# Kernel optimization log

Hardware: AMD Instinct MI355X
Metric: run time of the kernel (lower is better)

## Reference

```python
import jax, jax.numpy as jnp
import numpy as np

EMBED = 2048
MLP = 8192
EPS = 1e-5


def setup_inputs() -> dict:
    key = jax.random.key(0)
    ks = jax.random.split(key, 16)
    s = 0.02
    inp = {
        "x": jax.random.normal(ks[0], (2, 2048, EMBED), dtype=jnp.float32),
        "wq": jax.random.normal(ks[1], (EMBED, EMBED), dtype=jnp.float32) * s,
        "bq": jnp.zeros((EMBED,), jnp.float32),
        "wk": jax.random.normal(ks[2], (EMBED, EMBED), dtype=jnp.float32) * s,
        "bk": jnp.zeros((EMBED,), jnp.float32),
        "wv": jax.random.normal(ks[3], (EMBED, EMBED), dtype=jnp.float32) * s,
        "bv": jnp.zeros((EMBED,), jnp.float32),
        "wd": jax.random.normal(ks[4], (EMBED, EMBED), dtype=jnp.float32) * s,
        "bd": jnp.zeros((EMBED,), jnp.float32),
        "ln_g": jnp.ones((EMBED,), jnp.float32),
        "ln_b": jnp.zeros((EMBED,), jnp.float32),
        "w1": jax.random.normal(ks[5], (MLP, EMBED), dtype=jnp.float32) * s,
        "b1": jnp.zeros((MLP,), jnp.float32),
        "w2": jax.random.normal(ks[6], (EMBED, MLP), dtype=jnp.float32) * s,
        "b2": jnp.zeros((EMBED,), jnp.float32),
    }
    return inp


def _layernorm(x, g, b):
    mu = jnp.mean(x, axis=-1, keepdims=True)
    var = jnp.mean(jnp.square(x - mu), axis=-1, keepdims=True)
    return (x - mu) * jax.lax.rsqrt(var + EPS) * g + b


def reference(x, wq, bq, wk, bk, wv, bv, wd, bd, ln_g, ln_b, w1, b1, w2, b2):
    # Single-head attention; scale uses full embed_dim (rotary_emb.dim == embed_dim).
    q = jnp.einsum("bse,fe->bsf", x, wq) + bq
    k = jnp.einsum("bse,fe->bsf", x, wk) + bk
    v = jnp.einsum("bse,fe->bsf", x, wv) + bv
    scores = jnp.einsum("bqe,bke->bqk", q, k) / jnp.sqrt(jnp.float32(EMBED))
    probs = jax.nn.softmax(scores, axis=-1)
    ctx = jnp.einsum("bqk,bke->bqe", probs, v)
    attn_out = jnp.einsum("bse,fe->bsf", ctx, wd) + bd
    # residual (dropout is identity in eval mode)
    h = x + attn_out
    h = _layernorm(h, ln_g, ln_b)
    mlp = jnp.einsum("bse,fe->bsf", h, w1) + b1
    mlp = jax.nn.gelu(mlp, approximate=False)
    mlp = jnp.einsum("bsf,ef->bse", mlp, w2) + b2
    return h + mlp
```

## Files before the change

kernel.cpp:

```cpp
#include <hip/hip_runtime.h>
#include <math.h>


#define SEQ 2048
#define EMB 2048
#define MLPD 8192

typedef __attribute__((ext_vector_type(8))) short short8;
typedef __attribute__((ext_vector_type(4))) float floatx4;
typedef unsigned short ushort;

__device__ __forceinline__ short f2bf(float f) {
  union { float f; unsigned u; } v; v.f = f;
  unsigned r = v.u + 0x7FFFu + ((v.u >> 16) & 1u);
  return (short)(r >> 16);
}

__device__ __forceinline__ void gload16(const ushort* g, ushort* l) {
  __builtin_amdgcn_global_load_lds(
      (__attribute__((address_space(1))) void*)g,
      (__attribute__((address_space(3))) void*)(unsigned)(unsigned long)l,
      16, 0, 0);
}

enum { EPI_QKV = 0, EPI_SCORES = 1, EPI_PV = 2, EPI_RES = 3, EPI_GELU = 4 };

template<int EPI>
__global__ __launch_bounds__(512, 2)
void gemm256(const ushort* __restrict__ A, const ushort* __restrict__ B,
             const float* __restrict__ bias, void* __restrict__ Cp,
             int N, int K, int lda, int ldb, int ldc,
             long sA, long sB, long sC, float scale)
{
  extern __shared__ ushort lds[];
  const int t = threadIdx.x;
  const int lane = t & 63, w = t >> 6;
  const int wm = w >> 2, wn = w & 3;
  const long bm = (long)blockIdx.y * 256;
  const long bn = (long)blockIdx.x * 256;
  A += (long)blockIdx.z * sA;
  B += (long)blockIdx.z * sB;

  const int srow = (w << 3) + (lane >> 3);
  const int gcol = (lane & 7) ^ ((lane >> 3) & 7);
  const ushort* Ag = A + (bm + srow) * (long)lda + gcol * 8;
  const ushort* Bg = B + (bn + srow) * (long)ldb + gcol * 8;
  ushort* lw = lds + (w << 9);

#define STAGE(gb, ld, dst, kk) do {                         \
    const ushort* _g = (gb) + (kk);                         \
    gload16(_g, lw + (dst));                                \
    gload16(_g + 64L * (ld), lw + (dst) + 4096); } while (0)

  const int l15 = lane & 15, q = lane >> 4, swz = l15 & 7;
  const int kx0 = (q ^ swz) << 3;
  const int kx1 = ((4 + q) ^ swz) << 3;
  const int arow = (wm << 13) + l15 * 64;
  const int brow = 16384 + ((wn >> 1) << 13) + ((wn & 1) << 12) + l15 * 64;

  floatx4 acc[8][4];
#pragma unroll
  for (int m = 0; m < 8; ++m)
#pragma unroll
    for (int n = 0; n < 4; ++n) acc[m][n] = (floatx4)0.0f;

  const int NT = K >> 6;

  STAGE(Ag,              lda, 0,     0);
  STAGE(Ag + 128L * lda, lda, 8192,  0);
  STAGE(Bg,              ldb, 16384, 0);
  STAGE(Bg + 128L * ldb, ldb, 24576, 0);
  STAGE(Ag,              lda, 32768, 64);
  asm volatile("s_waitcnt vmcnt(2)" ::: "memory");
  __builtin_amdgcn_s_barrier();

  for (int kt = 0; kt < NT; ++kt) {
    const int buf  = (kt & 1) ? 32768 : 0;
    const int bufn = 32768 - buf;
    const long k1 = (long)((kt + 1 < NT) ? kt + 1 : NT - 1) << 6;
    const long k2 = (long)((kt + 2 < NT) ? kt + 2 : NT - 1) << 6;
    short8 a0[4], a1[4], b0[4], b1[4];

#pragma unroll
    for (int mf = 0; mf < 4; ++mf) {
      a0[mf] = *(const short8*)&lds[buf + arow + mf * 1024 + kx0];
      a1[mf] = *(const short8*)&lds[buf + arow + mf * 1024 + kx1];
    }
#pragma unroll
    for (int nf = 0; nf < 2; ++nf) {
      b0[nf] = *(const short8*)&lds[buf + brow + nf * 1024 + kx0];
      b1[nf] = *(const short8*)&lds[buf + brow + nf * 1024 + kx1];
    }
    STAGE(Ag + 128L * lda, lda, bufn + 8192, k1);
    __builtin_amdgcn_s_barrier();
    asm volatile("s_waitcnt lgkmcnt(0)");
    __builtin_amdgcn_s_setprio(1);
#pragma unroll
    for (int mf = 0; mf < 4; ++mf)
#pragma unroll
      for (int nf = 0; nf < 2; ++nf) {
        acc[mf][nf] = __builtin_amdgcn_mfma_f32_16x16x32_bf16(a0[mf], b0[nf], acc[mf][nf], 0, 0, 0);
        acc[mf][nf] = __builtin_amdgcn_mfma_f32_16x16x32_bf16(a1[mf], b1[nf], acc[mf][nf], 0, 0, 0);
      }
    __builtin_amdgcn_s_setprio(0);
    __builtin_amdgcn_s_barrier();

#pragma unroll
    for (int nf = 2; nf < 4; ++nf) {
      b0[nf] = *(const short8*)&lds[buf + brow + nf * 1024 + kx0];
      b1[nf] = *(const short8*)&lds[buf + brow + nf * 1024 + kx1];
    }
    STAGE(Bg, ldb, bufn + 16384, k1);
    __builtin_amdgcn_s_barrier();
    asm volatile("s_waitcnt lgkmcnt(0)");
    __builtin_amdgcn_s_setprio(1);
#pragma unroll
    for (int mf = 0; mf < 4; ++mf)
#pragma unroll
      for (int nf = 2; nf < 4; ++nf) {
        acc[mf][nf] = __builtin_amdgcn_mfma_f32_16x16x32_bf16(a0[mf], b0[nf], acc[mf][nf], 0, 0, 0);
        acc[mf][nf] = __builtin_amdgcn_mfma_f32_16x16x32_bf16(a1[mf], b1[nf], acc[mf][nf], 0, 0, 0);
      }
    __builtin_amdgcn_s_setprio(0);
    __builtin_amdgcn_s_barrier();

#pragma unroll
    for (int mf = 0; mf < 4; ++mf) {
      a0[mf] = *(const short8*)&lds[buf + arow + (4 + mf) * 1024 + kx0];
      a1[mf] = *(const short8*)&lds[buf + arow + (4 + mf) * 1024 + kx1];
    }
    STAGE(Bg + 128L * ldb, ldb, bufn + 24576, k1);
    __builtin_amdgcn_s_barrier();
    asm volatile("s_waitcnt lgkmcnt(0)");
    __builtin_amdgcn_s_setprio(1);
#pragma unroll
    for (int mf = 0; mf < 4; ++mf)
#pragma unroll
      for (int nf = 0; nf < 2; ++nf) {
        acc[4 + mf][nf] = __builtin_amdgcn_mfma_f32_16x16x32_bf16(a0[mf], b0[nf], acc[4 + mf][nf], 0, 0, 0);
        acc[4 + mf][nf] = __builtin_amdgcn_mfma_f32_16x16x32_bf16(a1[mf], b1[nf], acc[4 + mf][nf], 0, 0, 0);
      }
    __builtin_amdgcn_s_setprio(0);
    __builtin_amdgcn_s_barrier();

    STAGE(Ag, lda, buf, k2);
    __builtin_amdgcn_s_barrier();
    __builtin_amdgcn_s_setprio(1);
#pragma unroll
    for (int mf = 0; mf < 4; ++mf)
#pragma unroll
      for (int nf = 2; nf < 4; ++nf) {
        acc[4 + mf][nf] = __builtin_amdgcn_mfma_f32_16x16x32_bf16(a0[mf], b0[nf], acc[4 + mf][nf], 0, 0, 0);
        acc[4 + mf][nf] = __builtin_amdgcn_mfma_f32_16x16x32_bf16(a1[mf], b1[nf], acc[4 + mf][nf], 0, 0, 0);
      }
    __builtin_amdgcn_s_setprio(0);
    asm volatile("s_waitcnt vmcnt(2)" ::: "memory");
    __builtin_amdgcn_s_barrier();
  }
#undef STAGE

  const int lq = lane >> 4;
#pragma unroll
  for (int mf = 0; mf < 8; ++mf) {
#pragma unroll
    for (int nf = 0; nf < 4; ++nf) {
#pragma unroll
      for (int i = 0; i < 4; ++i) {
        const long r = bm + wm * 128 + mf * 16 + lq * 4 + i;
        const long c = bn + wn * 64 + nf * 16 + l15;
        float val = acc[mf][nf][i];
        if constexpr (EPI == EPI_QKV) {
          val += bias[c];
          ((ushort*)Cp)[r * (long)ldc + c] = (ushort)f2bf(val);
        } else if constexpr (EPI == EPI_SCORES) {
          ((float*)Cp)[(long)blockIdx.z * sC + r * (long)ldc + c] = val * scale;
        } else {
          val += bias[c];
          float g = 0.5f * val * (1.0f + erff(val * 0.70710678118f));
          ((ushort*)Cp)[r * (long)ldc + c] = (ushort)f2bf(g);
        }
      }
    }
  }
}

template<int EPI>
__global__ __launch_bounds__(256)
void gemm_bt(const ushort* __restrict__ A, const ushort* __restrict__ B,
             const float* __restrict__ bias, const float* __restrict__ res,
             void* __restrict__ Cp, int N, int K,
             int lda, int ldb, int ldc,
             long sA, long sB, long sC, float scale)
{
  __shared__ ushort As[128 * 32];
  __shared__ ushort Bs[128 * 32];

  const int t = threadIdx.x;
  const int lane = t & 63, wid = t >> 6;
  const int wm = wid >> 1, wn = wid & 1;
  const long bm = (long)blockIdx.y * 128;
  const long bn = (long)blockIdx.x * 128;
  A += (long)blockIdx.z * sA;
  B += (long)blockIdx.z * sB;

  const int srow = (wid << 5) + (lane >> 2);
  const int scol = (lane & 3) << 3;
  const ushort* a0 = A + (bm + srow) * (long)lda + scol;
  const ushort* a1 = a0 + 16L * lda;
  const ushort* b0 = B + (bn + srow) * (long)ldb + scol;
  const ushort* b1 = b0 + 16L * ldb;
  ushort* lA0 = As + (wid << 10);
  ushort* lA1 = lA0 + 512;
  ushort* lB0 = Bs + (wid << 10);
  ushort* lB1 = lB0 + 512;

  floatx4 acc[4][4];
#pragma unroll
  for (int m = 0; m < 4; ++m)
#pragma unroll
    for (int n = 0; n < 4; ++n) acc[m][n] = (floatx4)0.0f;

  const int l15 = lane & 15, kq = (lane >> 4) << 3;
  const int abase = ((wm << 6) + l15) * 32 + kq;
  const int bbase = ((wn << 6) + l15) * 32 + kq;

  for (int kb = 0; kb < K; kb += 32) {
    gload16(a0 + kb, lA0);
    gload16(a1 + kb, lA1);
    gload16(b0 + kb, lB0);
    gload16(b1 + kb, lB1);
    __syncthreads();

    short8 a[4], b[4];
#pragma unroll
    for (int m = 0; m < 4; ++m)
      a[m] = *reinterpret_cast<const short8*>(&As[abase + m * (16 * 32)]);
#pragma unroll
    for (int n = 0; n < 4; ++n)
      b[n] = *reinterpret_cast<const short8*>(&Bs[bbase + n * (16 * 32)]);
#pragma unroll
    for (int m = 0; m < 4; ++m)
#pragma unroll
      for (int n = 0; n < 4; ++n)
        acc[m][n] = __builtin_amdgcn_mfma_f32_16x16x32_bf16(a[m], b[n], acc[m][n], 0, 0, 0);
    __syncthreads();
  }

  const int lq = lane >> 4;
#pragma unroll
  for (int m = 0; m < 4; ++m) {
#pragma unroll
    for (int n = 0; n < 4; ++n) {
#pragma unroll
      for (int i = 0; i < 4; ++i) {
        const long r = bm + wm * 64 + m * 16 + lq * 4 + i;
        const long c = bn + wn * 64 + n * 16 + l15;
        float val = acc[m][n][i];
        if constexpr (EPI == EPI_SCORES) {
          ((float*)Cp)[(long)blockIdx.z * sC + r * (long)ldc + c] = val * scale;
        } else if constexpr (EPI == EPI_PV) {
          ((ushort*)Cp)[(long)blockIdx.z * sC + r * (long)ldc + c] = (ushort)f2bf(val);
        }
      }
    }
  }
}

__global__ __launch_bounds__(256)
void reduce2(const float* __restrict__ p0, const float* __restrict__ p1,
             const float* __restrict__ bias, const float* __restrict__ res,
             float* __restrict__ out)
{
  const long i = ((long)blockIdx.x * 256 + threadIdx.x) * 8;
  const int c = (int)(i & 2047);
  float4 a0 = *(const float4*)(p0 + i),  a1 = *(const float4*)(p0 + i + 4);
  float4 q0 = *(const float4*)(p1 + i),  q1 = *(const float4*)(p1 + i + 4);
  float4 r0 = *(const float4*)(res + i), r1 = *(const float4*)(res + i + 4);
  float4 b0 = *(const float4*)(bias + c), b1 = *(const float4*)(bias + c + 4);
  float4 o0 = {a0.x + q0.x + r0.x + b0.x, a0.y + q0.y + r0.y + b0.y,
               a0.z + q0.z + r0.z + b0.z, a0.w + q0.w + r0.w + b0.w};
  float4 o1 = {a1.x + q1.x + r1.x + b1.x, a1.y + q1.y + r1.y + b1.y,
               a1.z + q1.z + r1.z + b1.z, a1.w + q1.w + r1.w + b1.w};
  *(float4*)(out + i) = o0;
  *(float4*)(out + i + 4) = o1;
}

__global__ __launch_bounds__(256)
void cvt8(const float* __restrict__ s, ushort* __restrict__ d) {
  const long i = ((long)blockIdx.x * 256 + threadIdx.x) * 8;
  float4 a = *reinterpret_cast<const float4*>(s + i);
  float4 b = *reinterpret_cast<const float4*>(s + i + 4);
  short8 v;
  v[0] = f2bf(a.x); v[1] = f2bf(a.y); v[2] = f2bf(a.z); v[3] = f2bf(a.w);
  v[4] = f2bf(b.x); v[5] = f2bf(b.y); v[6] = f2bf(b.z); v[7] = f2bf(b.w);
  *reinterpret_cast<short8*>(d + i) = v;
}

__global__ __launch_bounds__(256)
void concat3(const float* __restrict__ b0, const float* __restrict__ b1,
             const float* __restrict__ b2, float* __restrict__ dst) {
  const int i = blockIdx.x * 256 + threadIdx.x;
  dst[i] = (i < 2048) ? b0[i] : (i < 4096) ? b1[i - 2048] : b2[i - 4096];
}

__global__ __launch_bounds__(256)
void transpose_v(const ushort* __restrict__ qkv, ushort* __restrict__ vT) {
  __shared__ ushort tile[32][33];
  const int b = blockIdx.z;
  const int s0 = blockIdx.x * 32, e0 = blockIdx.y * 32;
  const int tx = threadIdx.x & 31, ty = threadIdx.x >> 5;
#pragma unroll
  for (int i = 0; i < 4; ++i) {
    const long s = (long)b * SEQ + s0 + ty + i * 8;
    tile[ty + i * 8][tx] = qkv[s * 6144 + 4096 + e0 + tx];
  }
  __syncthreads();
#pragma unroll
  for (int i = 0; i < 4; ++i) {
    const long e = (long)b * SEQ + e0 + ty + i * 8;
    vT[e * SEQ + s0 + tx] = tile[tx][ty + i * 8];
  }
}

__global__ __launch_bounds__(256)
void softmax_rows(const float* __restrict__ S, ushort* __restrict__ P) {
  const long row = blockIdx.x;
  const float* src = S + row * 2048;
  const int t = threadIdx.x, lane = t & 63, wid = t >> 6;
  float4 a = *reinterpret_cast<const float4*>(src + t * 8);
  float4 b = *reinterpret_cast<const float4*>(src + t * 8 + 4);
  float v[8] = {a.x, a.y, a.z, a.w, b.x, b.y, b.z, b.w};
  float m = v[0];
#pragma unroll
  for (int i = 1; i < 8; ++i) m = fmaxf(m, v[i]);
#pragma unroll
  for (int o = 32; o; o >>= 1) m = fmaxf(m, __shfl_xor(m, o));
  __shared__ float rm[4], rs[4];
  if (!lane) rm[wid] = m;
  __syncthreads();
  m = fmaxf(fmaxf(rm[0], rm[1]), fmaxf(rm[2], rm[3]));
  float e[8], s = 0.f;
#pragma unroll
  for (int i = 0; i < 8; ++i) { e[i] = __expf(v[i] - m); s += e[i]; }
#pragma unroll
  for (int o = 32; o; o >>= 1) s += __shfl_xor(s, o);
  if (!lane) rs[wid] = s;
  __syncthreads();
  s = rs[0] + rs[1] + rs[2] + rs[3];
  const float inv = 1.0f / s;
  short8 wv;
#pragma unroll
  for (int i = 0; i < 8; ++i) wv[i] = f2bf(e[i] * inv);
  *reinterpret_cast<short8*>(P + row * 2048 + t * 8) = wv;
}

__global__ __launch_bounds__(256)
void layernorm_rows(const float* __restrict__ X, const float* __restrict__ g,
                    const float* __restrict__ bb, float* __restrict__ H,
                    ushort* __restrict__ Hb) {
  const long row = blockIdx.x;
  const float* src = X + row * 2048;
  const int t = threadIdx.x, lane = t & 63, wid = t >> 6;
  float4 a = *reinterpret_cast<const float4*>(src + t * 8);
  float4 b = *reinterpret_cast<const float4*>(src + t * 8 + 4);
  float v[8] = {a.x, a.y, a.z, a.w, b.x, b.y, b.z, b.w};
  float s = 0.f, ss = 0.f;
#pragma unroll
  for (int i = 0; i < 8; ++i) { s += v[i]; ss += v[i] * v[i]; }
#pragma unroll
  for (int o = 32; o; o >>= 1) { s += __shfl_xor(s, o); ss += __shfl_xor(ss, o); }
  __shared__ float r1[4], r2[4];
  if (!lane) { r1[wid] = s; r2[wid] = ss; }
  __syncthreads();
  s = r1[0] + r1[1] + r1[2] + r1[3];
  ss = r2[0] + r2[1] + r2[2] + r2[3];
  const float mu = s * (1.0f / 2048.0f);
  const float var = ss * (1.0f / 2048.0f) - mu * mu;
  const float inv = rsqrtf(var + 1e-5f);
  float o0[8];
  short8 wv;
#pragma unroll
  for (int i = 0; i < 8; ++i) {
    const int c = t * 8 + i;
    o0[i] = (v[i] - mu) * inv * g[c] + bb[c];
    wv[i] = f2bf(o0[i]);
  }
  float4 w0 = {o0[0], o0[1], o0[2], o0[3]}, w1 = {o0[4], o0[5], o0[6], o0[7]};
  *reinterpret_cast<float4*>(H + row * 2048 + t * 8) = w0;
  *reinterpret_cast<float4*>(H + row * 2048 + t * 8 + 4) = w1;
  *reinterpret_cast<short8*>(Hb + row * 2048 + t * 8) = wv;
}

extern "C" void kernel_launch(void* const* d_in, const int* in_sizes, int n_in,
                              void* d_out, int out_size, void* d_ws, size_t ws_size,
                              hipStream_t stream) {
  const float* x    = (const float*)d_in[0];
  const float* wq   = (const float*)d_in[1];
  const float* bq   = (const float*)d_in[2];
  const float* wk   = (const float*)d_in[3];
  const float* bk   = (const float*)d_in[4];
  const float* wv   = (const float*)d_in[5];
  const float* bv   = (const float*)d_in[6];
  const float* wd   = (const float*)d_in[7];
  const float* bd   = (const float*)d_in[8];
  const float* ln_g = (const float*)d_in[9];
  const float* ln_b = (const float*)d_in[10];
  const float* w1   = (const float*)d_in[11];
  const float* b1   = (const float*)d_in[12];
  const float* w2   = (const float*)d_in[13];
  const float* b2   = (const float*)d_in[14];
  float* out = (float*)d_out;

  (void)hipFuncSetAttribute((const void*)&gemm256<EPI_QKV>,
      hipFuncAttributeMaxDynamicSharedMemorySize, 131072);
  (void)hipFuncSetAttribute((const void*)&gemm256<EPI_GELU>,
      hipFuncAttributeMaxDynamicSharedMemorySize, 131072);
  (void)hipFuncSetAttribute((const void*)&gemm256<EPI_SCORES>,
      hipFuncAttributeMaxDynamicSharedMemorySize, 131072);

  char* p = (char*)d_ws;
  const size_t MB = 1048576;
  ushort* wdb    = (ushort*)(p + 0 * MB);
  ushort* w1b    = (ushort*)(p + 8 * MB);
  ushort* w2b    = (ushort*)(p + 40 * MB);
  float*  bqkv   = (float*) (p + 72 * MB);
  ushort* xb     = (ushort*)(p + 73 * MB);
  ushort* probs  = xb;
  ushort* qkv    = (ushort*)(p + 89 * MB);
  float*  partA  = (float*) (p + 89 * MB);
  ushort* mlpb   = (ushort*)(p + 89 * MB);
  ushort* vT     = (ushort*)(p + 137 * MB);
  ushort* wqkvb  = (ushort*)(p + 153 * MB);
  float*  scores = (float*) (p + 153 * MB);
  ushort* ctx    = (ushort*)(p + 153 * MB);
  float*  tres   = (float*) (p + 153 * MB);
  float*  partM0 = (float*) (p + 0 * MB);
  float*  h      = (float*) (p + 185 * MB);
  ushort* hb     = (ushort*)(p + 217 * MB);

  const dim3 blk(256), blk512(512);
  const long SQ = (long)SEQ * SEQ;

  cvt8<<<4096, blk, 0, stream>>>(x, xb);
  cvt8<<<2048, blk, 0, stream>>>(wq, wqkvb);
  cvt8<<<2048, blk, 0, stream>>>(wk, wqkvb + 4194304);
  cvt8<<<2048, blk, 0, stream>>>(wv, wqkvb + 8388608);
  cvt8<<<2048, blk, 0, stream>>>(wd, wdb);
  cvt8<<<8192, blk, 0, stream>>>(w1, w1b);
  cvt8<<<8192, blk, 0, stream>>>(w2, w2b);
  concat3<<<24, blk, 0, stream>>>(bq, bk, bv, bqkv);

  gemm256<EPI_QKV><<<dim3(24, 16, 1), blk512, 131072, stream>>>(
      xb, wqkvb, bqkv, qkv, 6144, 2048, 2048, 2048, 6144, 0, 0, 0, 1.f);

  transpose_v<<<dim3(64, 64, 2), blk, 0, stream>>>(qkv, vT);

  gemm_bt<EPI_SCORES><<<dim3(16, 16, 2), blk, 0, stream>>>(
      qkv, qkv + 2048, nullptr, nullptr, scores, 2048, 2048, 6144, 6144, 2048,
      2048L * 6144, 2048L * 6144, SQ, 0.022097086912079608f);

  softmax_rows<<<dim3(4096), blk, 0, stream>>>(scores, probs);

  gemm_bt<EPI_PV><<<dim3(16, 16, 2), blk, 0, stream>>>(
      probs, vT, nullptr, nullptr, ctx, 2048, 2048, 2048, 2048, 2048,
      SQ, SQ, SQ, 1.f);

  gemm256<EPI_SCORES><<<dim3(8, 16, 2), blk512, 131072, stream>>>(
      ctx, wdb, nullptr, partA, 2048, 1024, 2048, 2048, 2048,
      1024, 1024, 8388608, 1.f);
  reduce2<<<4096, blk, 0, stream>>>(partA, partA + 8388608, bd, x, tres);

  layernorm_rows<<<4096, blk, 0, stream>>>(tres, ln_g, ln_b, h, hb);

  gemm256<EPI_GELU><<<dim3(32, 16, 1), blk512, 131072, stream>>>(
      hb, w1b, b1, mlpb, 8192, 2048, 2048, 2048, 8192, 0, 0, 0, 1.f);

  gemm256<EPI_SCORES><<<dim3(8, 16, 2), blk512, 131072, stream>>>(
      mlpb, w2b, nullptr, partM0, 2048, 4096, 8192, 8192, 2048,
      4096, 4096, (long)(153 * MB / 4), 1.f);
  reduce2<<<4096, blk, 0, stream>>>(partM0, (float*)(p + 153 * MB), b2, h, out);
}
```

Baseline: 686.2 us.

## Remap GEMM tiles across XCDs, deepen B prefetch, fuse reduce into layernorm

The gemm256 kernel now remaps block IDs so consecutive work tiles land on the same XCD, aiming for better L2 reuse. It also reorders the staging schedule so B tiles are prefetched two k-steps ahead and one barrier per iteration is dropped. The split-K reduction for the attention output projection is fused into the layernorm kernel, which removes one launch and one full-tensor round trip through memory. The deeper prefetch changes the vmcnt waits and buffer reuse ordering, so any ordering mistake could corrupt the shared-memory tiles.

```diff
diff --git a/kernel.cpp b/kernel.cpp
--- a/kernel.cpp
+++ b/kernel.cpp
@@ -36,8 +36,13 @@
   const int t = threadIdx.x;
   const int lane = t & 63, w = t >> 6;
   const int wm = w >> 2, wn = w & 3;
-  const long bm = (long)blockIdx.y * 256;
-  const long bn = (long)blockIdx.x * 256;
+
+  const int gx = gridDim.x, gy = gridDim.y;
+  const int bid = blockIdx.y * gx + blockIdx.x;
+  const int cpx = (gx * gy) >> 3;
+  const int work = (bid & 7) * cpx + (bid >> 3);
+  const long bm = (long)(work % gy) * 256;
+  const long bn = (long)(work / gy) * 256;
   A += (long)blockIdx.z * sA;
   B += (long)blockIdx.z * sB;
 
@@ -70,28 +75,32 @@
   STAGE(Ag + 128L * lda, lda, 8192,  0);
   STAGE(Bg,              ldb, 16384, 0);
   STAGE(Bg + 128L * ldb, ldb, 24576, 0);
-  STAGE(Ag,              lda, 32768, 64);
-  asm volatile("s_waitcnt vmcnt(2)" ::: "memory");
+  {
+    const long k1p = (NT > 1) ? 64 : 0;
+    STAGE(Bg,              ldb, 32768 + 16384, k1p);
+    STAGE(Bg + 128L * ldb, ldb, 32768 + 24576, k1p);
+  }
+  asm volatile("s_waitcnt vmcnt(4)" ::: "memory");
   __builtin_amdgcn_s_barrier();
 
   for (int kt = 0; kt < NT; ++kt) {
-    const int buf  = (kt & 1) ? 32768 : 0;
-    const int bufn = 32768 - buf;
+    const int cur = (kt & 1) ? 32768 : 0;
+    const int nxt = 32768 - cur;
     const long k1 = (long)((kt + 1 < NT) ? kt + 1 : NT - 1) << 6;
     const long k2 = (long)((kt + 2 < NT) ? kt + 2 : NT - 1) << 6;
     short8 a0[4], a1[4], b0[4], b1[4];
 
 #pragma unroll
     for (int mf = 0; mf < 4; ++mf) {
-      a0[mf] = *(const short8*)&lds[buf + arow + mf * 1024 + kx0];
-      a1[mf] = *(const short8*)&lds[buf + arow + mf * 1024 + kx1];
+      a0[mf] = *(const short8*)&lds[cur + arow + mf * 1024 + kx0];
+      a1[mf] = *(const short8*)&lds[cur + arow + mf * 1024 + kx1];
     }
 #pragma unroll
     for (int nf = 0; nf < 2; ++nf) {
-      b0[nf] = *(const short8*)&lds[buf + brow + nf * 1024 + kx0];
-      b1[nf] = *(const short8*)&lds[buf + brow + nf * 1024 + kx1];
+      b0[nf] = *(const short8*)&lds[cur + brow + nf * 1024 + kx0];
+      b1[nf] = *(const short8*)&lds[cur + brow + nf * 1024 + kx1];
     }
-    STAGE(Ag + 128L * lda, lda, bufn + 8192, k1);
+    STAGE(Ag, lda, nxt, k1);
     __builtin_amdgcn_s_barrier();
     asm volatile("s_waitcnt lgkmcnt(0)");
     __builtin_amdgcn_s_setprio(1);
@@ -107,10 +116,10 @@
 
 #pragma unroll
     for (int nf = 2; nf < 4; ++nf) {
-      b0[nf] = *(const short8*)&lds[buf + brow + nf * 1024 + kx0];
-      b1[nf] = *(const short8*)&lds[buf + brow + nf * 1024 + kx1];
+      b0[nf] = *(const short8*)&lds[cur + brow + nf * 1024 + kx0];
+      b1[nf] = *(const short8*)&lds[cur + brow + nf * 1024 + kx1];
     }
-    STAGE(Bg, ldb, bufn + 16384, k1);
+    STAGE(Ag + 128L * lda, lda, nxt + 8192, k1);
     __builtin_amdgcn_s_barrier();
     asm volatile("s_waitcnt lgkmcnt(0)");
     __builtin_amdgcn_s_setprio(1);
@@ -126,10 +135,10 @@
 
 #pragma unroll
     for (int mf = 0; mf < 4; ++mf) {
-      a0[mf] = *(const short8*)&lds[buf + arow + (4 + mf) * 1024 + kx0];
-      a1[mf] = *(const short8*)&lds[buf + arow + (4 + mf) * 1024 + kx1];
+      a0[mf] = *(const short8*)&lds[cur + arow + (4 + mf) * 1024 + kx0];
+      a1[mf] = *(const short8*)&lds[cur + arow + (4 + mf) * 1024 + kx1];
     }
-    STAGE(Bg + 128L * ldb, ldb, bufn + 24576, k1);
+    STAGE(Bg, ldb, cur + 16384, k2);
     __builtin_amdgcn_s_barrier();
     asm volatile("s_waitcnt lgkmcnt(0)");
     __builtin_amdgcn_s_setprio(1);
@@ -143,8 +152,7 @@
     __builtin_amdgcn_s_setprio(0);
     __builtin_amdgcn_s_barrier();
 
-    STAGE(Ag, lda, buf, k2);
-    __builtin_amdgcn_s_barrier();
+    STAGE(Bg + 128L * ldb, ldb, cur + 24576, k2);
     __builtin_amdgcn_s_setprio(1);
 #pragma unroll
     for (int mf = 0; mf < 4; ++mf)
@@ -154,7 +162,7 @@
         acc[4 + mf][nf] = __builtin_amdgcn_mfma_f32_16x16x32_bf16(a1[mf], b1[nf], acc[4 + mf][nf], 0, 0, 0);
       }
     __builtin_amdgcn_s_setprio(0);
-    asm volatile("s_waitcnt vmcnt(2)" ::: "memory");
+    asm volatile("s_waitcnt vmcnt(4)" ::: "memory");
     __builtin_amdgcn_s_barrier();
   }
 #undef STAGE
@@ -355,40 +363,51 @@
 }
 
 __global__ __launch_bounds__(256)
-void layernorm_rows(const float* __restrict__ X, const float* __restrict__ g,
-                    const float* __restrict__ bb, float* __restrict__ H,
-                    ushort* __restrict__ Hb) {
+void layernorm_fused(const float* __restrict__ p0, const float* __restrict__ p1,
+                     const float* __restrict__ bias, const float* __restrict__ res,
+                     const float* __restrict__ g, const float* __restrict__ bb,
+                     float* __restrict__ H, ushort* __restrict__ Hb) {
   const long row = blockIdx.x;
-  const float* src = X + row * 2048;
+  const long base = row * 2048;
   const int t = threadIdx.x, lane = t & 63, wid = t >> 6;
-  float4 a = *reinterpret_cast<const float4*>(src + t * 8);
-  float4 b = *reinterpret_cast<const float4*>(src + t * 8 + 4);
-  float v[8] = {a.x, a.y, a.z, a.w, b.x, b.y, b.z, b.w};
+  const long i = base + t * 8;
+  const int c0 = t * 8;
+  float v[8];
+  {
+    float4 a0 = *(const float4*)(p0 + i),  a1 = *(const float4*)(p0 + i + 4);
+    float4 q0 = *(const float4*)(p1 + i),  q1 = *(const float4*)(p1 + i + 4);
+    float4 r0 = *(const float4*)(res + i), r1 = *(const float4*)(res + i + 4);
+    float4 b0 = *(const float4*)(bias + c0), b1 = *(const float4*)(bias + c0 + 4);
+    v[0] = a0.x + q0.x + r0.x + b0.x; v[1] = a0.y + q0.y + r0.y + b0.y;
+    v[2] = a0.z + q0.z + r0.z + b0.z; v[3] = a0.w + q0.w + r0.w + b0.w;
+    v[4] = a1.x + q1.x + r1.x + b1.x; v[5] = a1.y + q1.y + r1.y + b1.y;
+    v[6] = a1.z + q1.z + r1.z + b1.z; v[7] = a1.w + q1.w + r1.w + b1.w;
+  }
   float s = 0.f, ss = 0.f;
 #pragma unroll
-  for (int i = 0; i < 8; ++i) { s += v[i]; ss += v[i] * v[i]; }
+  for (int i2 = 0; i2 < 8; ++i2) { s += v[i2]; ss += v[i2] * v[i2]; }
 #pragma unroll
   for (int o = 32; o; o >>= 1) { s += __shfl_xor(s, o); ss += __shfl_xor(ss, o); }
-  __shared__ float r1[4], r2[4];
-  if (!lane) { r1[wid] = s; r2[wid] = ss; }
+  __shared__ float r1s[4], r2s[4];
+  if (!lane) { r1s[wid] = s; r2s[wid] = ss; }
   __syncthreads();
-  s = r1[0] + r1[1] + r1[2] + r1[3];
-  ss = r2[0] + r2[1] + r2[2] + r2[3];
+  s = r1s[0] + r1s[1] + r1s[2] + r1s[3];
+  ss = r2s[0] + r2s[1] + r2s[2] + r2s[3];
   const float mu = s * (1.0f / 2048.0f);
   const float var = ss * (1.0f / 2048.0f) - mu * mu;
   const float inv = rsqrtf(var + 1e-5f);
   float o0[8];
   short8 wv;
 #pragma unroll
-  for (int i = 0; i < 8; ++i) {
-    const int c = t * 8 + i;
-    o0[i] = (v[i] - mu) * inv * g[c] + bb[c];
-    wv[i] = f2bf(o0[i]);
+  for (int i2 = 0; i2 < 8; ++i2) {
+    const int c = c0 + i2;
+    o0[i2] = (v[i2] - mu) * inv * g[c] + bb[c];
+    wv[i2] = f2bf(o0[i2]);
   }
   float4 w0 = {o0[0], o0[1], o0[2], o0[3]}, w1 = {o0[4], o0[5], o0[6], o0[7]};
-  *reinterpret_cast<float4*>(H + row * 2048 + t * 8) = w0;
-  *reinterpret_cast<float4*>(H + row * 2048 + t * 8 + 4) = w1;
-  *reinterpret_cast<short8*>(Hb + row * 2048 + t * 8) = wv;
+  *reinterpret_cast<float4*>(H + i) = w0;
+  *reinterpret_cast<float4*>(H + i + 4) = w1;
+  *reinterpret_cast<short8*>(Hb + i) = wv;
 }
 
 extern "C" void kernel_launch(void* const* d_in, const int* in_sizes, int n_in,
@@ -433,8 +452,8 @@
   ushort* wqkvb  = (ushort*)(p + 153 * MB);
   float*  scores = (float*) (p + 153 * MB);
   ushort* ctx    = (ushort*)(p + 153 * MB);
-  float*  tres   = (float*) (p + 153 * MB);
   float*  partM0 = (float*) (p + 0 * MB);
+  float*  partM1 = (float*) (p + 153 * MB);
   float*  h      = (float*) (p + 185 * MB);
   ushort* hb     = (ushort*)(p + 217 * MB);
 
@@ -468,9 +487,9 @@
   gemm256<EPI_SCORES><<<dim3(8, 16, 2), blk512, 131072, stream>>>(
       ctx, wdb, nullptr, partA, 2048, 1024, 2048, 2048, 2048,
       1024, 1024, 8388608, 1.f);
-  reduce2<<<4096, blk, 0, stream>>>(partA, partA + 8388608, bd, x, tres);
-
-  layernorm_rows<<<4096, blk, 0, stream>>>(tres, ln_g, ln_b, h, hb);
+
+  layernorm_fused<<<4096, blk, 0, stream>>>(
+      partA, partA + 8388608, bd, x, ln_g, ln_b, h, hb);
 
   gemm256<EPI_GELU><<<dim3(32, 16, 1), blk512, 131072, stream>>>(
       hb, w1b, b1, mlpb, 8192, 2048, 2048, 2048, 8192, 0, 0, 0, 1.f);
@@ -478,5 +497,5 @@
   gemm256<EPI_SCORES><<<dim3(8, 16, 2), blk512, 131072, stream>>>(
       mlpb, w2b, nullptr, partM0, 2048, 4096, 8192, 8192, 2048,
       4096, 4096, (long)(153 * MB / 4), 1.f);
-  reduce2<<<4096, blk, 0, stream>>>(partM0, (float*)(p + 153 * MB), b2, h, out);
-}
+  reduce2<<<4096, blk, 0, stream>>>(partM0, partM1, b2, h, out);
+}
```

Result: no change. 673.0 us (-1.9%).
